# Kernel optimization log

Measured on AMD Instinct MI355X. Metric: run time of the kernel, lower is better.

Reference implementation:

```python
import jax, jax.numpy as jnp
import numpy as np
import math

B, N_TOK, C, H = 8, 1024, 384, 6
K, S, P = 3, 2, 1
OUT_C, HID = 384, 4 * 384
EPS = 1e-5
NEG_INF = float('-inf')


def _build_conv_mask(num_token, k, s, p):
    """Replicates ConvAttentionMask (include_cls_token=True). Returns (mask[(N+2),(N+2)], idx[(W,k^2)] with -1 for padding)."""
    I = int(math.sqrt(num_token))
    ref = np.arange(num_token).reshape(I, I)
    ref = np.pad(ref, ((0, p), (0, p)), constant_values=-1)
    cent = np.arange(k // 2 - p, I - k // 2 + p, s)
    cc = np.stack(np.meshgrid(cent, cent, indexing='ij'), -1).reshape(-1, 1, 2)  # cartesian_prod order
    ke = np.arange(-(k // 2), k // 2 + 1)
    kc = np.stack(np.meshgrid(ke, ke, indexing='ij'), -1).reshape(1, -1, 2)
    coords = cc + kc  # (W, k^2, 2); negative coords wrap like torch fancy indexing -> hit -1 padding
    idx = ref[coords[..., 0], coords[..., 1]]  # (W, k^2)
    mask = np.full((num_token, num_token), NEG_INF, np.float32)
    for w in idx:
        v = w[w >= 0]
        mask[np.ix_(v, v)] = 1.0
    idx = idx + (idx >= 0).astype(np.int32)  # shift for cls token; -1 stays -1
    mask = np.pad(mask, ((1, 0), (1, 0)), constant_values=1.0)  # cls row/col
    mask = np.pad(mask, ((0, 1), (0, 1)), constant_values=0.0)  # extra zero-padded token
    return mask, idx

MASK_NP, IDX_NP = _build_conv_mask(N_TOK, K, S, P)
W_WIN = IDX_NP.shape[0]
# torch negative index -1 on a length-(N_TOK+1) tensor -> wrap to last token
IDX_FLAT = np.where(IDX_NP < 0, IDX_NP + N_TOK + 1, IDX_NP).reshape(-1)


def _ln(x, w, b):
    mu = jnp.mean(x, -1, keepdims=True)
    var = jnp.mean(jnp.square(x - mu), -1, keepdims=True)
    return (x - mu) * jax.lax.rsqrt(var + EPS) * w + b


def setup_inputs() -> dict:
    key = jax.random.key(0)
    ks = jax.random.split(key, 8)
    sd = 0.02
    return {
        'x': jax.random.normal(ks[0], (B, N_TOK + 1, C), jnp.float32),
        'norm1_w': jnp.ones((C,), jnp.float32), 'norm1_b': jnp.zeros((C,), jnp.float32),
        'qkv_w': sd * jax.random.normal(ks[1], (3 * C, C), jnp.float32),
        'proj_w': sd * jax.random.normal(ks[2], (C, C), jnp.float32),
        'proj_b': jnp.zeros((C,), jnp.float32),
        'norm2_w': jnp.ones((C,), jnp.float32), 'norm2_b': jnp.zeros((C,), jnp.float32),
        'pool_w': sd * jax.random.normal(ks[3], (C, K * K * C), jnp.float32),
        'pool_b': jnp.zeros((C,), jnp.float32),
        'norm3_w': jnp.ones((C,), jnp.float32), 'norm3_b': jnp.zeros((C,), jnp.float32),
        'fc1_w': sd * jax.random.normal(ks[4], (HID, C), jnp.float32),
        'fc1_b': jnp.zeros((HID,), jnp.float32),
        'fc2_w': sd * jax.random.normal(ks[5], (OUT_C, HID), jnp.float32),
        'fc2_b': jnp.zeros((OUT_C,), jnp.float32),
    }


def reference(x, norm1_w, norm1_b, qkv_w, proj_w, proj_b, norm2_w, norm2_b,
              pool_w, pool_b, norm3_w, norm3_b, fc1_w, fc1_b, fc2_w, fc2_b):
    mask = jnp.asarray(MASK_NP)  # (N_TOK+2, N_TOK+2), values in {-inf, 0, 1}
    Bv, N, Cv = x.shape
    d = Cv // H
    h = _ln(x, norm1_w, norm1_b)
    h = jnp.pad(h, ((0, 0), (0, 1), (0, 0)))  # append zero token -> (B, N+1, C)
    M = N + 1
    # attention (scale = num_heads**-0.5 as in the source, qkv has no bias)
    qkv = (h @ qkv_w.T).reshape(Bv, M, 3, H, d).transpose(2, 0, 3, 1, 4)
    q, k, v = qkv[0], qkv[1], qkv[2]
    scores = jnp.einsum('bhqd,bhkd->bhqk', q, k) * (H ** -0.5)
    # multiplicative mask {-inf,0,1}: keep where 1, zero where 0, -inf where -inf (intended semantics)
    scores = jnp.where(mask == 1.0, scores, jnp.where(mask == 0.0, 0.0, NEG_INF))
    probs = jax.nn.softmax(scores, axis=-1)
    attn = jnp.einsum('bhqk,bhkd->bhqd', probs, v).transpose(0, 2, 1, 3).reshape(Bv, M, Cv)
    attn = attn @ proj_w.T + proj_b
    h = h + attn
    h = h[:, :-1, :]  # drop padded token -> (B, N, C)
    h = _ln(h, norm2_w, norm2_b)
    # conv-style pooling: gather k^2 tokens per window, project
    gathered = h[:, IDX_FLAT, :].reshape(Bv, W_WIN, K * K * Cv)
    tok = gathered @ pool_w.T + pool_b  # (B, W, C)
    h = jnp.concatenate([h[:, :1, :], tok], axis=1)  # prepend cls -> (B, W+1, C)
    h = _ln(h, norm3_w, norm3_b)
    h = jax.nn.gelu(h @ fc1_w.T + fc1_b, approximate=False)
    return h @ fc2_w.T + fc2_b  # (B, W+1, OUT_C)
```

## Files before the change

### kernel.cpp

```cpp
#include <hip/hip_runtime.h>


typedef unsigned short u16;
typedef unsigned int u32;
typedef short s16x8 __attribute__((ext_vector_type(8)));
typedef float f32x4 __attribute__((ext_vector_type(4)));

__device__ __forceinline__ float b2f(u16 u) {
    return __uint_as_float(((u32)u) << 16);
}
__device__ __forceinline__ u16 f2b(float f) {
    u32 u = __float_as_uint(f);
    return (u16)((u + 0x7FFFu + ((u >> 16) & 1u)) >> 16);
}
__device__ __forceinline__ float wave_sum(float v) {
#pragma unroll
    for (int o = 32; o > 0; o >>= 1) v += __shfl_xor(v, o, 64);
    return v;
}
__device__ __forceinline__ float wave_max(float v) {
#pragma unroll
    for (int o = 32; o > 0; o >>= 1) v = fmaxf(v, __shfl_xor(v, o, 64));
    return v;
}
__device__ __forceinline__ float dot8(const float* qsh, int d0, uint4 u) {
    return qsh[d0 + 0] * b2f((u16)(u.x)) + qsh[d0 + 1] * b2f((u16)(u.x >> 16)) +
           qsh[d0 + 2] * b2f((u16)(u.y)) + qsh[d0 + 3] * b2f((u16)(u.y >> 16)) +
           qsh[d0 + 4] * b2f((u16)(u.z)) + qsh[d0 + 5] * b2f((u16)(u.z >> 16)) +
           qsh[d0 + 6] * b2f((u16)(u.w)) + qsh[d0 + 7] * b2f((u16)(u.w >> 16));
}

#define CCH 384
#define SCALE 0.40824829046386302f
#define NEG_BIG (-1e30f)

__global__ __launch_bounds__(64) void ln1_pad(const float* __restrict__ x,
                                              const float* __restrict__ w,
                                              const float* __restrict__ bb,
                                              u16* __restrict__ h1) {
    int row = blockIdx.x;
    int t = row % 1026, b = row / 1026;
    int lane = threadIdx.x;
    u16* out = h1 + (size_t)row * CCH;
    if (t == 1025) {
#pragma unroll
        for (int i = 0; i < 6; i++) out[lane + 64 * i] = 0;
        return;
    }
    const float* in = x + ((size_t)b * 1025 + t) * CCH;
    float v[6];
    float s = 0.f, ss = 0.f;
#pragma unroll
    for (int i = 0; i < 6; i++) {
        v[i] = in[lane + 64 * i];
        s += v[i];
        ss += v[i] * v[i];
    }
    s = wave_sum(s);
    ss = wave_sum(ss);
    float mu = s * (1.f / 384.f);
    float var = ss * (1.f / 384.f) - mu * mu;
    float inv = rsqrtf(var + 1e-5f);
#pragma unroll
    for (int i = 0; i < 6; i++) {
        int c = lane + 64 * i;
        out[c] = f2b((v[i] - mu) * inv * w[c] + bb[c]);
    }
}

__global__ __launch_bounds__(64) void ln2_inplace(u16* __restrict__ h,
                                                  const float* __restrict__ w,
                                                  const float* __restrict__ bb) {
    int b = blockIdx.x / 1025, t = blockIdx.x % 1025;
    u16* p = h + ((size_t)b * 1026 + t) * CCH;
    int lane = threadIdx.x;
    float v[6];
    float s = 0.f, ss = 0.f;
#pragma unroll
    for (int i = 0; i < 6; i++) {
        v[i] = b2f(p[lane + 64 * i]);
        s += v[i];
        ss += v[i] * v[i];
    }
    s = wave_sum(s);
    ss = wave_sum(ss);
    float mu = s * (1.f / 384.f);
    float var = ss * (1.f / 384.f) - mu * mu;
    float inv = rsqrtf(var + 1e-5f);
#pragma unroll
    for (int i = 0; i < 6; i++) {
        int c = lane + 64 * i;
        p[c] = f2b((v[i] - mu) * inv * w[c] + bb[c]);
    }
}

__global__ __launch_bounds__(64) void ln3_concat(const u16* __restrict__ h2,
                                                 const float* __restrict__ tokf,
                                                 const float* __restrict__ w,
                                                 const float* __restrict__ bb,
                                                 u16* __restrict__ h3) {
    int row = blockIdx.x;
    int b = row / 257, t = row % 257;
    int lane = threadIdx.x;
    float v[6];
    if (t == 0) {
        const u16* in = h2 + (size_t)b * 1026 * CCH;
#pragma unroll
        for (int i = 0; i < 6; i++) v[i] = b2f(in[lane + 64 * i]);
    } else {
        const float* in = tokf + ((size_t)b * 256 + (t - 1)) * CCH;
#pragma unroll
        for (int i = 0; i < 6; i++) v[i] = in[lane + 64 * i];
    }
    float s = 0.f, ss = 0.f;
#pragma unroll
    for (int i = 0; i < 6; i++) {
        s += v[i];
        ss += v[i] * v[i];
    }
    s = wave_sum(s);
    ss = wave_sum(ss);
    float mu = s * (1.f / 384.f);
    float var = ss * (1.f / 384.f) - mu * mu;
    float inv = rsqrtf(var + 1e-5f);
    u16* out = h3 + (size_t)row * CCH;
#pragma unroll
    for (int i = 0; i < 6; i++) {
        int c = lane + 64 * i;
        out[c] = f2b((v[i] - mu) * inv * w[c] + bb[c]);
    }
}

template <bool GATHER, int SPLITK, bool BIAS, bool GELU_ACT, bool RES,
          bool ATOMIC>
__global__ __launch_bounds__(256) void gemm_mf(const u16* __restrict__ A,
                                               int lda,
                                               const float* __restrict__ Bw,
                                               const float* __restrict__ bias,
                                               const u16* __restrict__ Res,
                                               void* __restrict__ Yv, int M,
                                               int N, int K) {
    __shared__ u16 Asl[128 * 40];
    __shared__ u16 Bsl[64 * 40];
    const int tid = threadIdx.x;
    const int wave = tid >> 6, lane = tid & 63;
    const int quad = lane >> 4, l15 = lane & 15;
    const int m0 = blockIdx.y * 128, n0 = blockIdx.x * 64;
    const int kp = (SPLITK > 1) ? blockIdx.z : 0;
    const int KS = K / SPLITK;
    const int kbase = kp * KS;

    f32x4 acc[2][4];
#pragma unroll
    for (int i = 0; i < 2; i++)
#pragma unroll
        for (int j = 0; j < 4; j++) acc[i][j] = (f32x4){0.f, 0.f, 0.f, 0.f};

    for (int kt = 0; kt < KS; kt += 32) {
        const int kk = kbase + kt;
#pragma unroll
        for (int L = 0; L < 2; L++) {
            int linear = L * 256 + tid;
            int row = linear >> 2, seg = linear & 3;
            int kf = kk + seg * 8;
            const u16* src;
            if (GATHER) {
                int m = m0 + row;
                int b = m >> 8, w = m & 255;
                int j = kf / 384, rem = kf - j * 384;
                int pr = 2 * (w >> 4) + j / 3 - 1;
                int pc = 2 * (w & 15) + j % 3 - 1;
                int tok = (pr >= 0 && pr < 32 && pc >= 0 && pc < 32)
                              ? (32 * pr + pc + 1)
                              : 1024;
                src = A + ((size_t)b * 1026 + tok) * 384 + rem;
            } else {
                int m = m0 + row;
                if (m >= M) m = M - 1;
                src = A + (size_t)m * lda + kf;
            }
            *(uint4*)(&Asl[row * 40 + seg * 8]) = *(const uint4*)src;
        }
#pragma unroll
        for (int L = 0; L < 2; L++) {
            int linear = L * 256 + tid;
            int row = linear >> 3, seg = linear & 7;
            float4 f =
                *(const float4*)(Bw + (size_t)(n0 + row) * K + kk + seg * 4);
            u32 lo = (u32)f2b(f.x) | ((u32)f2b(f.y) << 16);
            u32 hi = (u32)f2b(f.z) | ((u32)f2b(f.w) << 16);
            *(uint2*)(&Bsl[row * 40 + seg * 4]) = make_uint2(lo, hi);
        }
        __syncthreads();
        s16x8 afr[2], bfr[4];
#pragma unroll
        for (int ms = 0; ms < 2; ms++)
            afr[ms] = *(const s16x8*)(&Asl[(wave * 32 + ms * 16 + l15) * 40 +
                                           quad * 8]);
#pragma unroll
        for (int ns = 0; ns < 4; ns++)
            bfr[ns] = *(const s16x8*)(&Bsl[(ns * 16 + l15) * 40 + quad * 8]);
#pragma unroll
        for (int ms = 0; ms < 2; ms++)
#pragma unroll
            for (int ns = 0; ns < 4; ns++)
                acc[ms][ns] = __builtin_amdgcn_mfma_f32_16x16x32_bf16(
                    afr[ms], bfr[ns], acc[ms][ns], 0, 0, 0);
        __syncthreads();
    }
#pragma unroll
    for (int ms = 0; ms < 2; ms++) {
#pragma unroll
        for (int ns = 0; ns < 4; ns++) {
            int n = n0 + ns * 16 + l15;
#pragma unroll
            for (int i = 0; i < 4; i++) {
                int m = m0 + wave * 32 + ms * 16 + quad * 4 + i;
                if (m >= M) continue;
                float v = acc[ms][ns][i];
                if (BIAS && (SPLITK == 1 || kp == 0)) v += bias[n];
                if (RES) v += b2f(Res[(size_t)m * N + n]);
                if (GELU_ACT) v = 0.5f * v * (1.f + erff(v * 0.70710678118f));
                if (ATOMIC)
                    atomicAdd((float*)Yv + (size_t)m * N + n, v);
                else
                    ((u16*)Yv)[(size_t)m * N + n] = f2b(v);
            }
        }
    }
}

__global__ __launch_bounds__(64) void attn_patch(u16* __restrict__ qkv) {
    int bid = blockIdx.x;
    int p = bid & 1023;
    int hb = bid >> 10;
    int h = hb % 6, b = hb / 6;
    int lane = threadIdx.x;
    int r = p >> 5, c = p & 31;
    int rlo, rhi, clo, chi;
    if (r & 1) { rlo = (r - 2 < 0) ? 0 : r - 2; rhi = (r + 2 > 31) ? 31 : r + 2; }
    else       { rlo = (r - 1 < 0) ? 0 : r - 1; rhi = (r + 1 > 31) ? 31 : r + 1; }
    if (c & 1) { clo = (c - 2 < 0) ? 0 : c - 2; chi = (c + 2 > 31) ? 31 : c + 2; }
    else       { clo = (c - 1 < 0) ? 0 : c - 1; chi = (c + 1 > 31) ? 31 : c + 1; }
    int nr = rhi - rlo + 1, nc = chi - clo + 1;
    int nk = nr * nc + 1;
    __shared__ int toks[64];
    __shared__ float qsh[64];
    int tok = 0;
    if (lane >= 1 && lane < nk) {
        int jj = lane - 1;
        tok = 1 + ((rlo + jj / nc) << 5) + (clo + jj % nc);
    }
    toks[lane] = tok;
    u16* base = qkv + (size_t)b * 1026 * 1152 + h * 64;
    qsh[lane] = b2f(base[(size_t)(1 + p) * 1152 + lane]);
    __syncthreads();
    float sc = NEG_BIG;
    if (lane < nk) {
        const u16* krow = base + (size_t)tok * 1152 + 384;
        float acc = 0.f;
#pragma unroll
        for (int d0 = 0; d0 < 64; d0 += 8)
            acc += dot8(qsh, d0, *(const uint4*)(krow + d0));
        sc = acc * SCALE;
    }
    float mx = fmaxf(wave_max(sc), 0.f);
    float pe = (lane < nk) ? expf(sc - mx) : 0.f;
    float Z = wave_sum(pe) + expf(-mx);
    float acc = 0.f;
    for (int j = 0; j < nk; j++) {
        float wj = __shfl(pe, j, 64);
        acc += wj * b2f(base[(size_t)toks[j] * 1152 + 768 + lane]);
    }
    base[(size_t)(1 + p) * 1152 + lane] = f2b(acc / Z);
}

__global__ __launch_bounds__(1024) void attn_cls(u16* __restrict__ qkv) {
    int h = blockIdx.x % 6, b = blockIdx.x / 6;
    u16* base = qkv + (size_t)b * 1026 * 1152 + h * 64;
    int tid = threadIdx.x, lane = tid & 63, wv = tid >> 6;
    __shared__ float sc[1026];
    __shared__ float qsh[64];
    __shared__ float redmax[16], redsum[16];
    __shared__ float pv[16][64];
    if (tid < 64) qsh[tid] = b2f(base[tid]);
    __syncthreads();
    for (int key = tid; key < 1026; key += 1024) {
        const u16* krow = base + (size_t)key * 1152 + 384;
        float acc = 0.f;
#pragma unroll
        for (int d0 = 0; d0 < 64; d0 += 8)
            acc += dot8(qsh, d0, *(const uint4*)(krow + d0));
        sc[key] = acc * SCALE;
    }
    __syncthreads();
    float lm = NEG_BIG;
    for (int key = tid; key < 1026; key += 1024) lm = fmaxf(lm, sc[key]);
    lm = wave_max(lm);
    if (lane == 0) redmax[wv] = lm;
    __syncthreads();
    float mx = NEG_BIG;
#pragma unroll
    for (int i = 0; i < 16; i++) mx = fmaxf(mx, redmax[i]);
    float lsum = 0.f;
    for (int key = tid; key < 1026; key += 1024) {
        float e = expf(sc[key] - mx);
        sc[key] = e;
        lsum += e;
    }
    lsum = wave_sum(lsum);
    if (lane == 0) redsum[wv] = lsum;
    __syncthreads();
    float Z = 0.f;
#pragma unroll
    for (int i = 0; i < 16; i++) Z += redsum[i];
    float acc = 0.f;
    for (int key = wv; key < 1026; key += 16)
        acc += sc[key] * b2f(base[(size_t)key * 1152 + 768 + lane]);
    pv[wv][lane] = acc;
    __syncthreads();
    if (tid < 64) {
        float s = 0.f;
#pragma unroll
        for (int w2 = 0; w2 < 16; w2++) s += pv[w2][tid];
        base[tid] = f2b(s / Z);
        base[(size_t)1025 * 1152 + tid] = 0;
    }
}

extern "C" void kernel_launch(void* const* d_in, const int* in_sizes, int n_in,
                              void* d_out, int out_size, void* d_ws,
                              size_t ws_size, hipStream_t stream) {
    const float* x      = (const float*)d_in[0];
    const float* n1w    = (const float*)d_in[1];
    const float* n1b    = (const float*)d_in[2];
    const float* qkv_w  = (const float*)d_in[3];
    const float* proj_w = (const float*)d_in[4];
    const float* proj_b = (const float*)d_in[5];
    const float* n2w    = (const float*)d_in[6];
    const float* n2b    = (const float*)d_in[7];
    const float* pool_w = (const float*)d_in[8];
    const float* pool_b = (const float*)d_in[9];
    const float* n3w    = (const float*)d_in[10];
    const float* n3b    = (const float*)d_in[11];
    const float* fc1_w  = (const float*)d_in[12];
    const float* fc1_b  = (const float*)d_in[13];
    const float* fc2_w  = (const float*)d_in[14];
    const float* fc2_b  = (const float*)d_in[15];

    u16* ws = (u16*)d_ws;
    u16* h1    = ws;
    u16* qkvb  = ws + 3151872;
    float* tokf = (float*)qkvb;
    u16* h3    = qkvb + 1572864;
    u16* mlp1  = qkvb + 2362368;

    hipMemsetAsync(d_out, 0, (size_t)2056 * 384 * 4, stream);

    ln1_pad<<<8 * 1026, 64, 0, stream>>>(x, n1w, n1b, h1);
    gemm_mf<false, 1, false, false, false, false>
        <<<dim3(1152 / 64, 65), 256, 0, stream>>>(h1, 384, qkv_w, nullptr,
                                                  nullptr, qkvb, 8208, 1152,
                                                  384);
    attn_patch<<<8 * 6 * 1024, 64, 0, stream>>>(qkvb);
    attn_cls<<<8 * 6, 1024, 0, stream>>>(qkvb);
    gemm_mf<false, 1, true, false, true, false>
        <<<dim3(384 / 64, 65), 256, 0, stream>>>(qkvb, 1152, proj_w, proj_b,
                                                 h1, h1, 8208, 384, 384);
    ln2_inplace<<<8 * 1025, 64, 0, stream>>>(h1, n2w, n2b);
    hipMemsetAsync(tokf, 0, (size_t)2048 * 384 * 4, stream);
    gemm_mf<true, 4, true, false, false, true>
        <<<dim3(384 / 64, 16, 4), 256, 0, stream>>>(h1, 384, pool_w, pool_b,
                                                    nullptr, tokf, 2048, 384,
                                                    3456);
    ln3_concat<<<8 * 257, 64, 0, stream>>>(h1, tokf, n3w, n3b, h3);
    gemm_mf<false, 1, true, true, false, false>
        <<<dim3(1536 / 64, 17), 256, 0, stream>>>(h3, 384, fc1_w, fc1_b,
                                                  nullptr, mlp1, 2056, 1536,
                                                  384);
    gemm_mf<false, 4, true, false, false, true>
        <<<dim3(384 / 64, 17, 4), 256, 0, stream>>>(mlp1, 1536, fc2_w, fc2_b,
                                                    nullptr, d_out, 2056, 384,
                                                    1536);
}
```

Before: 314.2 us.

## Process two query tokens per wave in patch attention; widen QKV GEMM tile

The patch-attention kernel now gives each 64-lane wave two query tokens, one per 32-lane half. Reductions run over half-waves, and keys and probabilities are broadcast with shuffles instead of through shared memory. This halves the block count and aims to use idle lanes, since each token has at most 26 keys. Separately, the GEMM gains a tile-width template parameter, and the QKV projection uses 128-wide N tiles to improve reuse of the A tile, at the cost of more accumulator registers.

```diff
diff --git a/kernel.cpp b/kernel.cpp
--- a/kernel.cpp
+++ b/kernel.cpp
@@ -21,6 +21,16 @@
 __device__ __forceinline__ float wave_max(float v) {
 #pragma unroll
     for (int o = 32; o > 0; o >>= 1) v = fmaxf(v, __shfl_xor(v, o, 64));
+    return v;
+}
+__device__ __forceinline__ float half_sum(float v) {
+#pragma unroll
+    for (int o = 16; o > 0; o >>= 1) v += __shfl_xor(v, o, 64);
+    return v;
+}
+__device__ __forceinline__ float half_max(float v) {
+#pragma unroll
+    for (int o = 16; o > 0; o >>= 1) v = fmaxf(v, __shfl_xor(v, o, 64));
     return v;
 }
 __device__ __forceinline__ float dot8(const float* qsh, int d0, uint4 u) {
@@ -131,7 +141,7 @@
     }
 }
 
-template <bool GATHER, int SPLITK, bool BIAS, bool GELU_ACT, bool RES,
+template <int TN, bool GATHER, int SPLITK, bool BIAS, bool GELU_ACT, bool RES,
           bool ATOMIC>
 __global__ __launch_bounds__(256) void gemm_mf(const u16* __restrict__ A,
                                                int lda,
@@ -141,20 +151,20 @@
                                                void* __restrict__ Yv, int M,
                                                int N, int K) {
     __shared__ u16 Asl[128 * 40];
-    __shared__ u16 Bsl[64 * 40];
+    __shared__ u16 Bsl[TN * 40];
     const int tid = threadIdx.x;
     const int wave = tid >> 6, lane = tid & 63;
     const int quad = lane >> 4, l15 = lane & 15;
-    const int m0 = blockIdx.y * 128, n0 = blockIdx.x * 64;
+    const int m0 = blockIdx.y * 128, n0 = blockIdx.x * TN;
     const int kp = (SPLITK > 1) ? blockIdx.z : 0;
     const int KS = K / SPLITK;
     const int kbase = kp * KS;
 
-    f32x4 acc[2][4];
+    f32x4 acc[2][TN / 16];
 #pragma unroll
     for (int i = 0; i < 2; i++)
 #pragma unroll
-        for (int j = 0; j < 4; j++) acc[i][j] = (f32x4){0.f, 0.f, 0.f, 0.f};
+        for (int j = 0; j < TN / 16; j++) acc[i][j] = (f32x4){0.f, 0.f, 0.f, 0.f};
 
     for (int kt = 0; kt < KS; kt += 32) {
         const int kk = kbase + kt;
@@ -182,7 +192,7 @@
             *(uint4*)(&Asl[row * 40 + seg * 8]) = *(const uint4*)src;
         }
 #pragma unroll
-        for (int L = 0; L < 2; L++) {
+        for (int L = 0; L < TN / 32; L++) {
             int linear = L * 256 + tid;
             int row = linear >> 3, seg = linear & 7;
             float4 f =
@@ -192,18 +202,18 @@
             *(uint2*)(&Bsl[row * 40 + seg * 4]) = make_uint2(lo, hi);
         }
         __syncthreads();
-        s16x8 afr[2], bfr[4];
+        s16x8 afr[2], bfr[TN / 16];
 #pragma unroll
         for (int ms = 0; ms < 2; ms++)
             afr[ms] = *(const s16x8*)(&Asl[(wave * 32 + ms * 16 + l15) * 40 +
                                            quad * 8]);
 #pragma unroll
-        for (int ns = 0; ns < 4; ns++)
+        for (int ns = 0; ns < TN / 16; ns++)
             bfr[ns] = *(const s16x8*)(&Bsl[(ns * 16 + l15) * 40 + quad * 8]);
 #pragma unroll
         for (int ms = 0; ms < 2; ms++)
 #pragma unroll
-            for (int ns = 0; ns < 4; ns++)
+            for (int ns = 0; ns < TN / 16; ns++)
                 acc[ms][ns] = __builtin_amdgcn_mfma_f32_16x16x32_bf16(
                     afr[ms], bfr[ns], acc[ms][ns], 0, 0, 0);
         __syncthreads();
@@ -211,7 +221,7 @@
 #pragma unroll
     for (int ms = 0; ms < 2; ms++) {
 #pragma unroll
-        for (int ns = 0; ns < 4; ns++) {
+        for (int ns = 0; ns < TN / 16; ns++) {
             int n = n0 + ns * 16 + l15;
 #pragma unroll
             for (int i = 0; i < 4; i++) {
@@ -232,10 +242,13 @@
 
 __global__ __launch_bounds__(64) void attn_patch(u16* __restrict__ qkv) {
     int bid = blockIdx.x;
-    int p = bid & 1023;
-    int hb = bid >> 10;
+    int idx = bid & 511;
+    int hb = bid >> 9;
     int h = hb % 6, b = hb / 6;
     int lane = threadIdx.x;
+    int hl = lane >> 5, l5 = lane & 31;
+    int p0 = idx * 2;
+    int p = p0 | hl;
     int r = p >> 5, c = p & 31;
     int rlo, rhi, clo, chi;
     if (r & 1) { rlo = (r - 2 < 0) ? 0 : r - 2; rhi = (r + 2 > 31) ? 31 : r + 2; }
@@ -244,35 +257,44 @@
     else       { clo = (c - 1 < 0) ? 0 : c - 1; chi = (c + 1 > 31) ? 31 : c + 1; }
     int nr = rhi - rlo + 1, nc = chi - clo + 1;
     int nk = nr * nc + 1;
-    __shared__ int toks[64];
-    __shared__ float qsh[64];
     int tok = 0;
-    if (lane >= 1 && lane < nk) {
-        int jj = lane - 1;
+    if (l5 >= 1 && l5 < nk) {
+        int jj = l5 - 1;
         tok = 1 + ((rlo + jj / nc) << 5) + (clo + jj % nc);
     }
-    toks[lane] = tok;
     u16* base = qkv + (size_t)b * 1026 * 1152 + h * 64;
-    qsh[lane] = b2f(base[(size_t)(1 + p) * 1152 + lane]);
+    __shared__ float qsh[2][64];
+    qsh[0][lane] = b2f(base[(size_t)(1 + p0) * 1152 + lane]);
+    qsh[1][lane] = b2f(base[(size_t)(2 + p0) * 1152 + lane]);
     __syncthreads();
     float sc = NEG_BIG;
-    if (lane < nk) {
+    if (l5 < nk) {
         const u16* krow = base + (size_t)tok * 1152 + 384;
         float acc = 0.f;
 #pragma unroll
         for (int d0 = 0; d0 < 64; d0 += 8)
-            acc += dot8(qsh, d0, *(const uint4*)(krow + d0));
+            acc += dot8(qsh[hl], d0, *(const uint4*)(krow + d0));
         sc = acc * SCALE;
     }
-    float mx = fmaxf(wave_max(sc), 0.f);
-    float pe = (lane < nk) ? expf(sc - mx) : 0.f;
-    float Z = wave_sum(pe) + expf(-mx);
-    float acc = 0.f;
-    for (int j = 0; j < nk; j++) {
+    float mx = fmaxf(half_max(sc), 0.f);
+    float pe = (l5 < nk) ? expf(sc - mx) : 0.f;
+    float Z = half_sum(pe) + expf(-mx);
+    int nk0 = __shfl(nk, 0, 64), nk1 = __shfl(nk, 32, 64);
+    float Z0 = __shfl(Z, 0, 64), Z1 = __shfl(Z, 32, 64);
+    float acc0 = 0.f;
+    for (int j = 0; j < nk0; j++) {
+        int t = __shfl(tok, j, 64);
         float wj = __shfl(pe, j, 64);
-        acc += wj * b2f(base[(size_t)toks[j] * 1152 + 768 + lane]);
-    }
-    base[(size_t)(1 + p) * 1152 + lane] = f2b(acc / Z);
+        acc0 += wj * b2f(base[(size_t)t * 1152 + 768 + lane]);
+    }
+    float acc1 = 0.f;
+    for (int j = 0; j < nk1; j++) {
+        int t = __shfl(tok, 32 + j, 64);
+        float wj = __shfl(pe, 32 + j, 64);
+        acc1 += wj * b2f(base[(size_t)t * 1152 + 768 + lane]);
+    }
+    base[(size_t)(1 + p0) * 1152 + lane] = f2b(acc0 / Z0);
+    base[(size_t)(2 + p0) * 1152 + lane] = f2b(acc1 / Z1);
 }
 
 __global__ __launch_bounds__(1024) void attn_cls(u16* __restrict__ qkv) {
@@ -358,27 +380,27 @@
     hipMemsetAsync(d_out, 0, (size_t)2056 * 384 * 4, stream);
 
     ln1_pad<<<8 * 1026, 64, 0, stream>>>(x, n1w, n1b, h1);
-    gemm_mf<false, 1, false, false, false, false>
-        <<<dim3(1152 / 64, 65), 256, 0, stream>>>(h1, 384, qkv_w, nullptr,
-                                                  nullptr, qkvb, 8208, 1152,
-                                                  384);
-    attn_patch<<<8 * 6 * 1024, 64, 0, stream>>>(qkvb);
+    gemm_mf<128, false, 1, false, false, false, false>
+        <<<dim3(1152 / 128, 65), 256, 0, stream>>>(h1, 384, qkv_w, nullptr,
+                                                   nullptr, qkvb, 8208, 1152,
+                                                   384);
+    attn_patch<<<8 * 6 * 512, 64, 0, stream>>>(qkvb);
     attn_cls<<<8 * 6, 1024, 0, stream>>>(qkvb);
-    gemm_mf<false, 1, true, false, true, false>
+    gemm_mf<64, false, 1, true, false, true, false>
         <<<dim3(384 / 64, 65), 256, 0, stream>>>(qkvb, 1152, proj_w, proj_b,
                                                  h1, h1, 8208, 384, 384);
     ln2_inplace<<<8 * 1025, 64, 0, stream>>>(h1, n2w, n2b);
     hipMemsetAsync(tokf, 0, (size_t)2048 * 384 * 4, stream);
-    gemm_mf<true, 4, true, false, false, true>
+    gemm_mf<64, true, 4, true, false, false, true>
         <<<dim3(384 / 64, 16, 4), 256, 0, stream>>>(h1, 384, pool_w, pool_b,
                                                     nullptr, tokf, 2048, 384,
                                                     3456);
     ln3_concat<<<8 * 257, 64, 0, stream>>>(h1, tokf, n3w, n3b, h3);
-    gemm_mf<false, 1, true, true, false, false>
+    gemm_mf<64, false, 1, true, true, false, false>
         <<<dim3(1536 / 64, 17), 256, 0, stream>>>(h3, 384, fc1_w, fc1_b,
                                                   nullptr, mlp1, 2056, 1536,
                                                   384);
-    gemm_mf<false, 4, true, false, false, true>
+    gemm_mf<64, false, 4, true, false, false, true>
         <<<dim3(384 / 64, 17, 4), 256, 0, stream>>>(mlp1, 1536, fc2_w, fc2_b,
                                                     nullptr, d_out, 2056, 384,
                                                     1536);
```

New measurement: 310.3 us. Within noise of the previous version (-1.2%).
